# Kernel tuning notes

Measured on AMD Instinct MI355X. Metric: run time of the kernel, lower is better.

The kernel has to match this reference:

```python
import jax, jax.numpy as jnp
import numpy as np

# Dimensions
B, C, H, L, NC = 2048, 64, 768, 2, 1000   # batch, contributors/task, hidden, num_labels, contributor pool
H2, H4 = H // 2, H // 4
RIN = H + H4  # reliability MLP input dim (fixes the declared-vs-fed shape bug in the source)


def setup_inputs() -> dict:
    key = jax.random.key(0)
    ks = jax.random.split(key, 16)
    w = lambda k, s: (jax.random.normal(k, s, dtype=jnp.float32) * 0.02)
    return {
        "task_embeddings": jax.random.normal(ks[0], (B, H), dtype=jnp.float32),
        "contributor_ids": jax.random.randint(ks[1], (B, C), 0, NC),
        "contributor_labels": jax.random.randint(ks[2], (B, C), -1, L),  # -1 = missing
        # reliability_estimation MLP: (H+H//4) -> H//2 -> H//4 -> 1
        "w1": w(ks[3], (RIN, H2)), "b1": jnp.zeros((H2,), jnp.float32),
        "w2": w(ks[4], (H2, H4)), "b2": jnp.zeros((H4,), jnp.float32),
        "w3": w(ks[5], (H4, 1)),  "b3": jnp.zeros((1,), jnp.float32),
        # task_difficulty_estimation MLP: H -> H//2 -> 1
        "d1": w(ks[6], (H, H2)), "db1": jnp.zeros((H2,), jnp.float32),
        "d2": w(ks[7], (H2, 1)), "db2": jnp.zeros((1,), jnp.float32),
        # contributor embeddings + reliability bias
        "emb_table": w(ks[8], (NC, H4)),
        "contrib_bias": jnp.zeros((NC,), jnp.float32),
    }


def reference(task_embeddings, contributor_ids, contributor_labels,
              w1, b1, w2, b2, w3, b3, d1, db1, d2, db2, emb_table, contrib_bias):
    # task difficulty: sigmoid(Linear(SiLU(Linear(x))))  -> [B, 1]
    task_difficulty = jax.nn.sigmoid(jax.nn.silu(task_embeddings @ d1 + db1) @ d2 + db2)

    # contributor reliability MLP on concat(task_embed, contributor_embed): [B, C, H+H//4]
    ce = emb_table[contributor_ids]                                  # [B, C, H4]
    te = jnp.broadcast_to(task_embeddings[:, None, :], (B, C, H))    # [B, C, H]
    combined = jnp.concatenate([te, ce], axis=-1)                    # [B, C, RIN]
    h = jax.nn.silu(combined @ w1 + b1)                              # dropout is eval-mode identity
    h = jax.nn.silu(h @ w2 + b2)
    est = jax.nn.sigmoid(h @ w3 + b3)[..., 0]                        # [B, C]
    bias = contrib_bias[contributor_ids]                             # [B, C]
    reliability_scores = jax.nn.sigmoid(est + bias)                  # double sigmoid, as in source

    # weighted label histogram (masked scatter-add via one-hot matmul)
    valid = (contributor_labels != -1)                               # [B, C]
    weight = reliability_scores * (1.0 - task_difficulty) * valid.astype(jnp.float32)
    one_hot = jax.nn.one_hot(jnp.clip(contributor_labels, 0, L - 1), L, dtype=jnp.float32)
    label_weights = jnp.einsum('bc,bcl->bl', weight, one_hot)        # [B, L]
    current_labels = jnp.argmax(label_weights, axis=1)               # [B]

    # reliability (hence labels) is iteration-invariant -> loop fixed point after 1 pass
    return (current_labels, reliability_scores)
```

## Files before the change

kernel.cpp:

```cpp
#include <hip/hip_runtime.h>
#include <math.h>

#define B_   2048
#define C_   64
#define H_   768
#define NC_  1000
#define H2_  384
#define H4_  192
#define RIN_ 960

using short8 = __attribute__((ext_vector_type(8))) short;
using f32x4  = __attribute__((ext_vector_type(4))) float;

__device__ __forceinline__ float silu_(float x){
    float e = __expf(-x);
    return x * __fdividef(1.f, 1.f + e);
}
__device__ __forceinline__ unsigned short f2bf_(float x){
    unsigned int u = __float_as_uint(x);
    u += 0x7fffu + ((u >> 16) & 1u);
    return (unsigned short)(u >> 16);
}
__device__ __forceinline__ unsigned short f2bft_(float x){
    return (unsigned short)(__float_as_uint(x) >> 16);
}
__device__ __forceinline__ float bf2f_(unsigned short h){
    return __uint_as_float(((unsigned int)h) << 16);
}

__global__ void k_sentinel(float* __restrict__ out, float code){ out[0] = code; }

__global__ __launch_bounds__(256) void k_w1split(const float* __restrict__ w1,
                                                 unsigned short* __restrict__ w1hi,
                                                 unsigned short* __restrict__ w1lo)
{
    const int idx = blockIdx.x * 256 + threadIdx.x;
    const int k = idx / H2_, j = idx - k * H2_;
    float x = w1[idx];
    unsigned short h = f2bf_(x);
    size_t dst = (size_t)(k >> 5) * (H2_ * 32) + (size_t)j * 32 + (k & 31);
    w1hi[dst] = h;
    w1lo[dst] = f2bft_(x - bf2f_(h));
}

#define CB_T1E_  256
#define CB_W2E_  544
#define CB_E1E_  1544
__global__ __launch_bounds__(256) void k_combo(const float* __restrict__ te,
                                               const float* __restrict__ w1,
                                               const float* __restrict__ w2,
                                               const float* __restrict__ emb,
                                               const int*   __restrict__ ids32,
                                               const unsigned short* __restrict__ w1hi,
                                               const unsigned short* __restrict__ w1lo,
                                               const float* __restrict__ b1,
                                               float* __restrict__ T1,
                                               unsigned short* __restrict__ w2hi,
                                               unsigned short* __restrict__ w2lo,
                                               float* __restrict__ E1,
                                               int* __restrict__ flag)
{
    __shared__ float er[H4_];
    __shared__ int any_nz;
    const int bb = blockIdx.x, t = threadIdx.x;

    if (bb < CB_T1E_) {
        const int bx = bb >> 1, by = bb & 1;
        const int b0 = bx * 16;
        const int jb = by * 192;
        const int w = t >> 6, l = t & 63;
        const int m = l & 15, g = l >> 4;
        const int row = b0 + m;

        f32x4 acc[3];
        #pragma unroll
        for (int jt = 0; jt < 3; ++jt) acc[jt] = (f32x4){0.f, 0.f, 0.f, 0.f};

        for (int ck = 0; ck < 24; ++ck) {
            const int kk = ck * 32;
            const float* pa = te + (size_t)row * H_ + kk + g * 8;
            float4 a0 = *(const float4*)pa;
            float4 a1 = *(const float4*)(pa + 4);
            float av[8] = {a0.x, a0.y, a0.z, a0.w, a1.x, a1.y, a1.z, a1.w};
            short8 ahi, alo;
            #pragma unroll
            for (int i = 0; i < 8; ++i) {
                unsigned short h = f2bf_(av[i]);
                ahi[i] = (short)h;
                alo[i] = (short)f2bft_(av[i] - bf2f_(h));
            }
            #pragma unroll
            for (int jt = 0; jt < 3; ++jt) {
                const int j = jb + w * 48 + jt * 16 + m;
                const size_t o = (size_t)ck * (H2_ * 32) + (size_t)j * 32 + g * 8;
                short8 bhi = *(const short8*)&w1hi[o];
                short8 blo = *(const short8*)&w1lo[o];
                acc[jt] = __builtin_amdgcn_mfma_f32_16x16x32_bf16(ahi, bhi, acc[jt], 0, 0, 0);
                acc[jt] = __builtin_amdgcn_mfma_f32_16x16x32_bf16(ahi, blo, acc[jt], 0, 0, 0);
                acc[jt] = __builtin_amdgcn_mfma_f32_16x16x32_bf16(alo, bhi, acc[jt], 0, 0, 0);
            }
        }
        #pragma unroll
        for (int jt = 0; jt < 3; ++jt) {
            const int j = jb + w * 48 + jt * 16 + m;
            const float bj = b1[j];
            #pragma unroll
            for (int reg = 0; reg < 4; ++reg)
                T1[(size_t)(b0 + g * 4 + reg) * H2_ + j] = acc[jt][reg] + bj;
        }
    } else if (bb < CB_W2E_) {
        const int idx = (bb - CB_T1E_) * 256 + t;
        const int k = idx / H4_, j = idx - k * H4_;
        float x = w2[idx];
        unsigned short h = f2bf_(x);
        size_t dst = (size_t)(k >> 5) * (H4_ * 32) + (size_t)j * 32 + (k & 31);
        w2hi[dst] = h;
        w2lo[dst] = f2bft_(x - bf2f_(h));
    } else if (bb < CB_E1E_) {
        const int id = bb - CB_W2E_;
        if (t < H4_) er[t] = emb[id * H4_ + t];
        __syncthreads();
        for (int k = t; k < H2_; k += 256) {
            float acc = 0.f;
            const float* wc = w1 + (size_t)H_ * H2_ + k;
            #pragma unroll 8
            for (int r = 0; r < H4_; ++r) acc += er[r] * wc[(size_t)r * H2_];
            E1[id * H2_ + k] = acc;
        }
    } else {
        if (t == 0) any_nz = 0;
        __syncthreads();
        int local = 0;
        for (int i = t; i < 2048; i += 256)
            if (ids32[2 * i + 1] != 0) { local = 1; break; }
        if (local) atomicOr(&any_nz, 1);
        __syncthreads();
        if (t == 0) flag[0] = (any_nz == 0) ? 1 : 0;
    }
}

#define HS_ 40
__global__ __launch_bounds__(256, 4) void k_main(const float* __restrict__ T1,
                                                 const float* __restrict__ E1,
                                                 const int*   __restrict__ ids,
                                                 const int*   __restrict__ labels,
                                                 const unsigned short* __restrict__ w2hi,
                                                 const unsigned short* __restrict__ w2lo,
                                                 const float* __restrict__ b2,
                                                 const float* __restrict__ w3,
                                                 const float* __restrict__ b3,
                                                 const float* __restrict__ cbias,
                                                 const int*   __restrict__ iflag,
                                                 float* __restrict__ out)
{
    __shared__ __align__(16) unsigned short h1hiS[C_ * HS_];
    __shared__ __align__(16) unsigned short h1loS[C_ * HS_];
    __shared__ __align__(16) float T1b[H2_];
    __shared__ float b2S[H4_], w3S[H4_];
    __shared__ int   ids_s[C_], lab_s[C_];
    __shared__ double sredS[4 * C_];

    const int b = blockIdx.x;
    const int t = threadIdx.x;
    const int l = t & 63, w = t >> 6;
    const int m = l & 15, g = l >> 4;
    const int kq0 = g * 8;

    if (t < C_) {
        if (iflag[0]) {
            ids_s[t] = (int)((const long long*)ids)[(size_t)b * C_ + t];
            lab_s[t] = (int)((const long long*)labels)[(size_t)b * C_ + t];
        } else {
            ids_s[t] = ids[b * C_ + t];
            lab_s[t] = labels[b * C_ + t];
        }
    }
    for (int k = t; k < H2_; k += 256) T1b[k] = T1[(size_t)b * H2_ + k];
    if (t < H4_) { b2S[t] = b2[t]; w3S[t] = w3[t]; }

    f32x4 acc[4][3];
    #pragma unroll
    for (int rt = 0; rt < 4; ++rt)
        #pragma unroll
        for (int jt = 0; jt < 3; ++jt) acc[rt][jt] = (f32x4){0.f, 0.f, 0.f, 0.f};

    __syncthreads();

    const int ck0 = b % 12;
    for (int ci = 0; ci < 12; ++ci) {
        int ck = ck0 + ci;
        if (ck >= 12) ck -= 12;
        const int kk = ck * 32;

        const unsigned short* gbh = w2hi + (size_t)ck * (H4_ * 32);
        const unsigned short* gbl = w2lo + (size_t)ck * (H4_ * 32);
        short8 bhi[3], blo[3];
        #pragma unroll
        for (int jt = 0; jt < 3; ++jt) {
            const int j = 48 * w + jt * 16 + m;
            bhi[jt] = *(const short8*)&gbh[j * 32 + kq0];
            blo[jt] = *(const short8*)&gbl[j * 32 + kq0];
        }

        #pragma unroll
        for (int it = 0; it < 2; ++it) {
            const int i  = t + it * 256;
            const int c  = i >> 3;
            const int kq = i & 7;
            float4 e  = *(const float4*)&E1[(size_t)ids_s[c] * H2_ + kk + kq * 4];
            float4 tv = *(const float4*)&T1b[kk + kq * 4];
            float x0 = silu_(tv.x + e.x), x1 = silu_(tv.y + e.y);
            float x2 = silu_(tv.z + e.z), x3 = silu_(tv.w + e.w);
            unsigned short h0 = f2bft_(x0), h1v = f2bft_(x1), h2v = f2bft_(x2), h3 = f2bft_(x3);
            uint2 uh, ul;
            uh.x = (unsigned)h0 | ((unsigned)h1v << 16);
            uh.y = (unsigned)h2v | ((unsigned)h3 << 16);
            ul.x = (unsigned)f2bft_(x0 - bf2f_(h0)) | ((unsigned)f2bft_(x1 - bf2f_(h1v)) << 16);
            ul.y = (unsigned)f2bft_(x2 - bf2f_(h2v)) | ((unsigned)f2bft_(x3 - bf2f_(h3)) << 16);
            *(uint2*)&h1hiS[c * HS_ + kq * 4] = uh;
            *(uint2*)&h1loS[c * HS_ + kq * 4] = ul;
        }
        __syncthreads();

        short8 ahi[4], alo[4];
        #pragma unroll
        for (int rt = 0; rt < 4; ++rt) {
            ahi[rt] = *(const short8*)&h1hiS[(rt * 16 + m) * HS_ + kq0];
            alo[rt] = *(const short8*)&h1loS[(rt * 16 + m) * HS_ + kq0];
        }
        #pragma unroll
        for (int jt = 0; jt < 3; ++jt) {
            #pragma unroll
            for (int rt = 0; rt < 4; ++rt) {
                acc[rt][jt] = __builtin_amdgcn_mfma_f32_16x16x32_bf16(ahi[rt], bhi[jt], acc[rt][jt], 0, 0, 0);
                acc[rt][jt] = __builtin_amdgcn_mfma_f32_16x16x32_bf16(ahi[rt], blo[jt], acc[rt][jt], 0, 0, 0);
                acc[rt][jt] = __builtin_amdgcn_mfma_f32_16x16x32_bf16(alo[rt], bhi[jt], acc[rt][jt], 0, 0, 0);
            }
        }
        __syncthreads();
    }

    double p[4][4];
    #pragma unroll
    for (int rt = 0; rt < 4; ++rt)
        #pragma unroll
        for (int reg = 0; reg < 4; ++reg) p[rt][reg] = 0.0;

    #pragma unroll
    for (int jt = 0; jt < 3; ++jt) {
        const int j = 48 * w + jt * 16 + m;
        const float bj = b2S[j];
        const double w3j = (double)w3S[j];
        #pragma unroll
        for (int rt = 0; rt < 4; ++rt)
            #pragma unroll
            for (int reg = 0; reg < 4; ++reg)
                p[rt][reg] += (double)silu_(acc[rt][jt][reg] + bj) * w3j;
    }
    #pragma unroll
    for (int rt = 0; rt < 4; ++rt)
        #pragma unroll
        for (int reg = 0; reg < 4; ++reg) {
            double v = p[rt][reg];
            v += __shfl_xor(v, 1);
            v += __shfl_xor(v, 2);
            v += __shfl_xor(v, 4);
            v += __shfl_xor(v, 8);
            p[rt][reg] = v;
        }
    if (m == 0) {
        #pragma unroll
        for (int rt = 0; rt < 4; ++rt)
            #pragma unroll
            for (int reg = 0; reg < 4; ++reg)
                sredS[w * C_ + rt * 16 + g * 4 + reg] = p[rt][reg];
    }
    __syncthreads();

    if (t < C_) {
        const int c = t;
        double s = sredS[c] + sredS[C_ + c] + sredS[2 * C_ + c] + sredS[3 * C_ + c];
        double est = 1.0 / (1.0 + exp(-(s + (double)b3[0])));
        double rel = 1.0 / (1.0 + exp(-(est + (double)cbias[ids_s[c]])));
        out[B_ + (size_t)b * C_ + c] = (float)rel;

        const int lb = lab_s[c];
        double mg = (lb == 1) ? rel : ((lb == 0) ? -rel : 0.0);
        #pragma unroll
        for (int o = 32; o > 0; o >>= 1) mg += __shfl_down(mg, o);
        if (t == 0) out[b] = (mg > 0.0) ? 1.0f : 0.0f;
    }
}

extern "C" void kernel_launch(void* const* d_in, const int* in_sizes, int n_in,
                              void* d_out, int out_size, void* d_ws, size_t ws_size,
                              hipStream_t stream)
{
    const float* te    = (const float*)d_in[0];
    const int*   ids   = (const int*)  d_in[1];
    const int*   labs  = (const int*)  d_in[2];
    const float* w1    = (const float*)d_in[3];
    const float* b1    = (const float*)d_in[4];
    const float* w2    = (const float*)d_in[5];
    const float* b2    = (const float*)d_in[6];
    const float* w3    = (const float*)d_in[7];
    const float* b3    = (const float*)d_in[8];
    const float* cbias = (const float*)d_in[14];
    const float* emb   = (const float*)d_in[13];
    float* out = (float*)d_out;

    const int expect[15] = {B_*H_, B_*C_, B_*C_, RIN_*H2_, H2_, H2_*H4_, H4_,
                            H4_, 1, H_*H2_, H2_, H2_, 1, NC_*H4_, NC_};
    if (n_in != 15) {
        k_sentinel<<<1, 1, 0, stream>>>(out, 3000.0f + (float)n_in);
        return;
    }
    for (int i = 0; i < 15; ++i) {
        if (in_sizes[i] != expect[i]) {
            k_sentinel<<<1, 1, 0, stream>>>(out, 2000.0f + 10.0f * (float)i);
            return;
        }
    }

    const size_t nE1 = (size_t)NC_ * H2_;
    const size_t nT1 = (size_t)B_ * H2_;
    const size_t nW1 = (size_t)RIN_ * H2_;
    const size_t nW2 = (size_t)H2_ * H4_;
    const size_t need = nE1 * 4 + nT1 * 4 + nW1 * 2 * 2 + nW2 * 2 * 2 + 16;
    if (ws_size < need) {
        k_sentinel<<<1, 1, 0, stream>>>(out, 1000.0f + (float)((double)ws_size / (1024.0 * 1024.0)));
        return;
    }
    float* ws = (float*)d_ws;
    float* E1 = ws;
    float* T1 = E1 + nE1;
    unsigned short* w1hi = (unsigned short*)(T1 + nT1);
    unsigned short* w1lo = w1hi + nW1;
    unsigned short* w2hi = w1lo + nW1;
    unsigned short* w2lo = w2hi + nW2;
    int* iflag = (int*)(w2lo + nW2);

    k_w1split<<<1152, 256, 0, stream>>>(w1, w1hi, w1lo);
    k_combo<<<CB_E1E_ + 1, 256, 0, stream>>>(te, w1, w2, emb, ids,
                                             w1hi, w1lo, b1, T1,
                                             w2hi, w2lo, E1, iflag);
    k_main<<<B_, 256, 0, stream>>>(T1, E1, ids, labs, w2hi, w2lo, b2, w3, b3, cbias, iflag, out);
}
```

Baseline: 121.1 us.

## Process two tasks per block to reuse W2 fragments across tasks

Each block of k_main now handles two batch rows instead of one, so every W2 hi/lo fragment loaded from global memory feeds MFMAs for both tasks. The launch grid is halved, and shared buffers and accumulators are doubled. This cuts W2 global traffic and per-block setup, at the cost of doubling accumulator registers and dropping the occupancy hint in launch bounds, which may reduce waves per CU. The epilogue now runs serially for the two tasks, with an extra barrier between them.

```diff
diff --git a/kernel.cpp b/kernel.cpp
--- a/kernel.cpp
+++ b/kernel.cpp
@@ -140,53 +140,60 @@
 }
 
 #define HS_ 40
-__global__ __launch_bounds__(256, 4) void k_main(const float* __restrict__ T1,
-                                                 const float* __restrict__ E1,
-                                                 const int*   __restrict__ ids,
-                                                 const int*   __restrict__ labels,
-                                                 const unsigned short* __restrict__ w2hi,
-                                                 const unsigned short* __restrict__ w2lo,
-                                                 const float* __restrict__ b2,
-                                                 const float* __restrict__ w3,
-                                                 const float* __restrict__ b3,
-                                                 const float* __restrict__ cbias,
-                                                 const int*   __restrict__ iflag,
-                                                 float* __restrict__ out)
+__global__ __launch_bounds__(256) void k_main(const float* __restrict__ T1,
+                                              const float* __restrict__ E1,
+                                              const int*   __restrict__ ids,
+                                              const int*   __restrict__ labels,
+                                              const unsigned short* __restrict__ w2hi,
+                                              const unsigned short* __restrict__ w2lo,
+                                              const float* __restrict__ b2,
+                                              const float* __restrict__ w3,
+                                              const float* __restrict__ b3,
+                                              const float* __restrict__ cbias,
+                                              const int*   __restrict__ iflag,
+                                              float* __restrict__ out)
 {
-    __shared__ __align__(16) unsigned short h1hiS[C_ * HS_];
-    __shared__ __align__(16) unsigned short h1loS[C_ * HS_];
-    __shared__ __align__(16) float T1b[H2_];
+    __shared__ __align__(16) unsigned short h1hiS[2][C_ * HS_];
+    __shared__ __align__(16) unsigned short h1loS[2][C_ * HS_];
+    __shared__ __align__(16) float T1b[2][H2_];
     __shared__ float b2S[H4_], w3S[H4_];
-    __shared__ int   ids_s[C_], lab_s[C_];
+    __shared__ int   ids_s[2][C_], lab_s[2][C_];
     __shared__ double sredS[4 * C_];
 
-    const int b = blockIdx.x;
+    const int b0 = blockIdx.x * 2;
     const int t = threadIdx.x;
     const int l = t & 63, w = t >> 6;
     const int m = l & 15, g = l >> 4;
     const int kq0 = g * 8;
 
-    if (t < C_) {
+    if (t < 2 * C_) {
+        const int task = t >> 6, c = t & 63;
+        const size_t off = (size_t)(b0 + task) * C_ + c;
         if (iflag[0]) {
-            ids_s[t] = (int)((const long long*)ids)[(size_t)b * C_ + t];
-            lab_s[t] = (int)((const long long*)labels)[(size_t)b * C_ + t];
+            ids_s[task][c] = (int)((const long long*)ids)[off];
+            lab_s[task][c] = (int)((const long long*)labels)[off];
         } else {
-            ids_s[t] = ids[b * C_ + t];
-            lab_s[t] = labels[b * C_ + t];
-        }
-    }
-    for (int k = t; k < H2_; k += 256) T1b[k] = T1[(size_t)b * H2_ + k];
+            ids_s[task][c] = ids[off];
+            lab_s[task][c] = labels[off];
+        }
+    }
+    for (int i = t; i < 2 * H2_; i += 256) {
+        int task = i / H2_, k = i - task * H2_;
+        T1b[task][k] = T1[(size_t)(b0 + task) * H2_ + k];
+    }
     if (t < H4_) { b2S[t] = b2[t]; w3S[t] = w3[t]; }
 
-    f32x4 acc[4][3];
+    f32x4 acc[2][4][3];
     #pragma unroll
-    for (int rt = 0; rt < 4; ++rt)
-        #pragma unroll
-        for (int jt = 0; jt < 3; ++jt) acc[rt][jt] = (f32x4){0.f, 0.f, 0.f, 0.f};
+    for (int s = 0; s < 2; ++s)
+        #pragma unroll
+        for (int rt = 0; rt < 4; ++rt)
+            #pragma unroll
+            for (int jt = 0; jt < 3; ++jt) acc[s][rt][jt] = (f32x4){0.f, 0.f, 0.f, 0.f};
 
     __syncthreads();
 
-    const int ck0 = b % 12;
+    const int ck0 = b0 % 12;
     for (int ci = 0; ci < 12; ++ci) {
         int ck = ck0 + ci;
         if (ck >= 12) ck -= 12;
@@ -203,12 +210,14 @@
         }
 
         #pragma unroll
-        for (int it = 0; it < 2; ++it) {
-            const int i  = t + it * 256;
-            const int c  = i >> 3;
-            const int kq = i & 7;
-            float4 e  = *(const float4*)&E1[(size_t)ids_s[c] * H2_ + kk + kq * 4];
-            float4 tv = *(const float4*)&T1b[kk + kq * 4];
+        for (int it = 0; it < 4; ++it) {
+            const int i    = t + it * 256;
+            const int task = i >> 9;
+            const int r    = i & 511;
+            const int c    = r >> 3;
+            const int kq   = r & 7;
+            float4 e  = *(const float4*)&E1[(size_t)ids_s[task][c] * H2_ + kk + kq * 4];
+            float4 tv = *(const float4*)&T1b[task][kk + kq * 4];
             float x0 = silu_(tv.x + e.x), x1 = silu_(tv.y + e.y);
             float x2 = silu_(tv.z + e.z), x3 = silu_(tv.w + e.w);
             unsigned short h0 = f2bft_(x0), h1v = f2bft_(x1), h2v = f2bft_(x2), h3 = f2bft_(x3);
@@ -217,78 +226,81 @@
             uh.y = (unsigned)h2v | ((unsigned)h3 << 16);
             ul.x = (unsigned)f2bft_(x0 - bf2f_(h0)) | ((unsigned)f2bft_(x1 - bf2f_(h1v)) << 16);
             ul.y = (unsigned)f2bft_(x2 - bf2f_(h2v)) | ((unsigned)f2bft_(x3 - bf2f_(h3)) << 16);
-            *(uint2*)&h1hiS[c * HS_ + kq * 4] = uh;
-            *(uint2*)&h1loS[c * HS_ + kq * 4] = ul;
-        }
-        __syncthreads();
-
-        short8 ahi[4], alo[4];
-        #pragma unroll
-        for (int rt = 0; rt < 4; ++rt) {
-            ahi[rt] = *(const short8*)&h1hiS[(rt * 16 + m) * HS_ + kq0];
-            alo[rt] = *(const short8*)&h1loS[(rt * 16 + m) * HS_ + kq0];
-        }
+            *(uint2*)&h1hiS[task][c * HS_ + kq * 4] = uh;
+            *(uint2*)&h1loS[task][c * HS_ + kq * 4] = ul;
+        }
+        __syncthreads();
+
+        #pragma unroll
+        for (int task = 0; task < 2; ++task) {
+            #pragma unroll
+            for (int rt = 0; rt < 4; ++rt) {
+                short8 ahi = *(const short8*)&h1hiS[task][(rt * 16 + m) * HS_ + kq0];
+                short8 alo = *(const short8*)&h1loS[task][(rt * 16 + m) * HS_ + kq0];
+                #pragma unroll
+                for (int jt = 0; jt < 3; ++jt) {
+                    acc[task][rt][jt] = __builtin_amdgcn_mfma_f32_16x16x32_bf16(ahi, bhi[jt], acc[task][rt][jt], 0, 0, 0);
+                    acc[task][rt][jt] = __builtin_amdgcn_mfma_f32_16x16x32_bf16(ahi, blo[jt], acc[task][rt][jt], 0, 0, 0);
+                    acc[task][rt][jt] = __builtin_amdgcn_mfma_f32_16x16x32_bf16(alo, bhi[jt], acc[task][rt][jt], 0, 0, 0);
+                }
+            }
+        }
+        __syncthreads();
+    }
+
+    #pragma unroll
+    for (int task = 0; task < 2; ++task) {
+        double p[4][4];
+        #pragma unroll
+        for (int rt = 0; rt < 4; ++rt)
+            #pragma unroll
+            for (int reg = 0; reg < 4; ++reg) p[rt][reg] = 0.0;
+
         #pragma unroll
         for (int jt = 0; jt < 3; ++jt) {
-            #pragma unroll
-            for (int rt = 0; rt < 4; ++rt) {
-                acc[rt][jt] = __builtin_amdgcn_mfma_f32_16x16x32_bf16(ahi[rt], bhi[jt], acc[rt][jt], 0, 0, 0);
-                acc[rt][jt] = __builtin_amdgcn_mfma_f32_16x16x32_bf16(ahi[rt], blo[jt], acc[rt][jt], 0, 0, 0);
-                acc[rt][jt] = __builtin_amdgcn_mfma_f32_16x16x32_bf16(alo[rt], bhi[jt], acc[rt][jt], 0, 0, 0);
+            const int j = 48 * w + jt * 16 + m;
+            const float bj = b2S[j];
+            const double w3j = (double)w3S[j];
+            #pragma unroll
+            for (int rt = 0; rt < 4; ++rt)
+                #pragma unroll
+                for (int reg = 0; reg < 4; ++reg)
+                    p[rt][reg] += (double)silu_(acc[task][rt][jt][reg] + bj) * w3j;
+        }
+        #pragma unroll
+        for (int rt = 0; rt < 4; ++rt)
+            #pragma unroll
+            for (int reg = 0; reg < 4; ++reg) {
+                double v = p[rt][reg];
+                v += __shfl_xor(v, 1);
+                v += __shfl_xor(v, 2);
+                v += __shfl_xor(v, 4);
+                v += __shfl_xor(v, 8);
+                p[rt][reg] = v;
             }
-        }
-        __syncthreads();
-    }
-
-    double p[4][4];
-    #pragma unroll
-    for (int rt = 0; rt < 4; ++rt)
-        #pragma unroll
-        for (int reg = 0; reg < 4; ++reg) p[rt][reg] = 0.0;
-
-    #pragma unroll
-    for (int jt = 0; jt < 3; ++jt) {
-        const int j = 48 * w + jt * 16 + m;
-        const float bj = b2S[j];
-        const double w3j = (double)w3S[j];
-        #pragma unroll
-        for (int rt = 0; rt < 4; ++rt)
-            #pragma unroll
-            for (int reg = 0; reg < 4; ++reg)
-                p[rt][reg] += (double)silu_(acc[rt][jt][reg] + bj) * w3j;
-    }
-    #pragma unroll
-    for (int rt = 0; rt < 4; ++rt)
-        #pragma unroll
-        for (int reg = 0; reg < 4; ++reg) {
-            double v = p[rt][reg];
-            v += __shfl_xor(v, 1);
-            v += __shfl_xor(v, 2);
-            v += __shfl_xor(v, 4);
-            v += __shfl_xor(v, 8);
-            p[rt][reg] = v;
-        }
-    if (m == 0) {
-        #pragma unroll
-        for (int rt = 0; rt < 4; ++rt)
-            #pragma unroll
-            for (int reg = 0; reg < 4; ++reg)
-                sredS[w * C_ + rt * 16 + g * 4 + reg] = p[rt][reg];
-    }
-    __syncthreads();
-
-    if (t < C_) {
-        const int c = t;
-        double s = sredS[c] + sredS[C_ + c] + sredS[2 * C_ + c] + sredS[3 * C_ + c];
-        double est = 1.0 / (1.0 + exp(-(s + (double)b3[0])));
-        double rel = 1.0 / (1.0 + exp(-(est + (double)cbias[ids_s[c]])));
-        out[B_ + (size_t)b * C_ + c] = (float)rel;
-
-        const int lb = lab_s[c];
-        double mg = (lb == 1) ? rel : ((lb == 0) ? -rel : 0.0);
-        #pragma unroll
-        for (int o = 32; o > 0; o >>= 1) mg += __shfl_down(mg, o);
-        if (t == 0) out[b] = (mg > 0.0) ? 1.0f : 0.0f;
+        if (m == 0) {
+            #pragma unroll
+            for (int rt = 0; rt < 4; ++rt)
+                #pragma unroll
+                for (int reg = 0; reg < 4; ++reg)
+                    sredS[w * C_ + rt * 16 + g * 4 + reg] = p[rt][reg];
+        }
+        __syncthreads();
+
+        if (t < C_) {
+            const int c = t;
+            double s = sredS[c] + sredS[C_ + c] + sredS[2 * C_ + c] + sredS[3 * C_ + c];
+            double est = 1.0 / (1.0 + exp(-(s + (double)b3[0])));
+            double rel = 1.0 / (1.0 + exp(-(est + (double)cbias[ids_s[task][c]])));
+            out[B_ + (size_t)(b0 + task) * C_ + c] = (float)rel;
+
+            const int lb = lab_s[task][c];
+            double mg = (lb == 1) ? rel : ((lb == 0) ? -rel : 0.0);
+            #pragma unroll
+            for (int o = 32; o > 0; o >>= 1) mg += __shfl_down(mg, o);
+            if (t == 0) out[b0 + task] = (mg > 0.0) ? 1.0f : 0.0f;
+        }
+        __syncthreads();
     }
 }
 
@@ -344,5 +356,5 @@
     k_combo<<<CB_E1E_ + 1, 256, 0, stream>>>(te, w1, w2, emb, ids,
                                              w1hi, w1lo, b1, T1,
                                              w2hi, w2lo, E1, iflag);
-    k_main<<<B_, 256, 0, stream>>>(T1, E1, ids, labs, w2hi, w2lo, b2, w3, b3, cbias, iflag, out);
-}
+    k_main<<<B_ / 2, 256, 0, stream>>>(T1, E1, ids, labs, w2hi, w2lo, b2, w3, b3, cbias, iflag, out);
+}
```

After: 176.3 us. +45.6%, slower.
